# Kernel optimization log

Hardware: AMD Instinct MI355X
Metric: run time of the kernel (lower is better)

The kernel has to match this reference:

```python
import jax, jax.numpy as jnp
import numpy as np

B, C, L = 32, 64, 4096
PS, STRIDE = 16, 8
PC = (L - PS) // STRIDE + 1  # 511
HID = 64


def setup_inputs() -> dict:
    key = jax.random.key(0)
    k = jax.random.split(key, 5)
    X = jax.random.normal(k[0], (B, C, L), dtype=jnp.float32)
    W1 = jax.random.normal(k[1], (HID, PS), dtype=jnp.float32) * 0.05  # Conv1d(1,64,PS) weight
    b1 = jax.random.normal(k[2], (HID,), dtype=jnp.float32) * 0.05
    W2 = jax.random.normal(k[3], (2, HID), dtype=jnp.float32) * 0.05   # Conv1d(64,2,1) weight
    b2 = jax.random.normal(k[4], (2,), dtype=jnp.float32) * 0.05
    return {"X": X, "W1": W1, "b1": b1, "W2": W2, "b2": b2}


def reference(X, W1, b1, W2, b2):
    Bn, Cn, Ln = X.shape
    s_bias = (PS - 1) / 2.0
    # anchors: center of each patch along the sequence axis
    anchor = jnp.arange(PC, dtype=X.dtype) * STRIDE + 0.5 * (PS - 1)  # (PC,)

    # ---- OffsetPredictor: unfold into (B, C, PC, PS) sliding windows ----
    idx = jnp.arange(PC)[:, None] * STRIDE + jnp.arange(PS)[None, :]  # (PC, PS)
    patches = X[:, :, idx]  # (B, C, PC, PS)
    # Conv1d(1, HID, PS) over a length-PS window == dense matmul with W1
    h = jax.nn.gelu(jnp.einsum('bcps,ks->bcpk', patches, W1) + b1, approximate=False)
    off = jnp.einsum('bcpk,jk->bcpj', h, W2) + b2  # (B, C, PC, 2)
    off = off.transpose(0, 2, 1, 3)  # (B, PC, C, 2)

    # ---- BoxCoder.decode ----
    dx = off[..., 0]
    ds = jax.nn.relu(off[..., 1] + s_bias)
    ref = anchor[None, :, None]
    lo = jnp.clip((dx + ref - ds) / (Ln - 1), 0.0, 1.0)  # (B, PC, C)
    hi = jnp.clip((dx + ref + ds) / (Ln - 1), 0.0, 1.0)

    # ---- BoxCoder.meshgrid: linear interp from box endpoints (align_corners) ----
    t = jnp.arange(PS, dtype=X.dtype) / (PS - 1)  # (PS,)
    xs = lo[..., None] + (hi - lo)[..., None] * t  # (B, PC, C, PS), in [0,1]
    ys = jnp.arange(Cn, dtype=X.dtype) / (Cn - 1)  # (C,), in [0,1]

    # ---- grid_sample(img=(B,1,C,L), grid=(xs,ys)*2-1, bilinear, align_corners=True) ----
    ix = xs * (Ln - 1)                                            # (B, PC, C, PS)
    iy = jnp.broadcast_to(ys[None, None, :, None] * (Cn - 1), ix.shape)
    ix0 = jnp.floor(ix)
    iy0 = jnp.floor(iy)
    wx = ix - ix0
    wy = iy - iy0
    ix0i = jnp.clip(ix0.astype(jnp.int32), 0, Ln - 1)
    ix1i = jnp.clip(ix0i + 1, 0, Ln - 1)
    iy0i = jnp.clip(iy0.astype(jnp.int32), 0, Cn - 1)
    iy1i = jnp.clip(iy0i + 1, 0, Cn - 1)

    gather = jax.vmap(lambda x, r, c: x[r, c])  # over batch; x:(C,L)
    v00 = gather(X, iy0i, ix0i)
    v01 = gather(X, iy0i, ix1i)
    v10 = gather(X, iy1i, ix0i)
    v11 = gather(X, iy1i, ix1i)
    out = (v00 * (1 - wx) + v01 * wx) * (1 - wy) + (v10 * (1 - wx) + v11 * wx) * wy
    # (B, PC, C, PS) -> (B, C, PC, PS)
    return out.transpose(0, 2, 1, 3)
```

## Files before the change

kernel.cpp:

```cpp
#include <hip/hip_runtime.h>
#include <math.h>

#define L_    4096
#define PS_   16
#define STR_  8
#define PC_   511
#define HID_  64
#define NBLK_ 2048

typedef __bf16 bf16x8 __attribute__((ext_vector_type(8)));
typedef float  f32x4  __attribute__((ext_vector_type(4)));

__device__ __forceinline__ float gelu_fast(float x) {
    float u = x * x;
    float t = fmaf(u, 0.10294294f, 2.3022082f);
    float a = x * t;
    float e = __builtin_amdgcn_exp2f(a);
    float r = __builtin_amdgcn_rcpf(e + 1.0f);
    return fmaf(-x, r, x);
}

__device__ __forceinline__ bf16x8 load_frag(const float* __restrict__ p) {
    float4 v0 = *reinterpret_cast<const float4*>(p);
    float4 v1 = *reinterpret_cast<const float4*>(p + 4);
    bf16x8 r;
    r[0] = (__bf16)v0.x; r[1] = (__bf16)v0.y; r[2] = (__bf16)v0.z; r[3] = (__bf16)v0.w;
    r[4] = (__bf16)v1.x; r[5] = (__bf16)v1.y; r[6] = (__bf16)v1.z; r[7] = (__bf16)v1.w;
    return r;
}

__global__ __launch_bounds__(256, 4) void depatch_kernel(
    const float* __restrict__ X,
    const float* __restrict__ W1,
    const float* __restrict__ b1,
    const float* __restrict__ W2,
    const float* __restrict__ b2,
    float* __restrict__ out)
{
    __shared__ __attribute__((aligned(16))) float s_row[L_ + 32];

    const int tid = threadIdx.x;
    const int bc  = blockIdx.x;
    const float* xrow = X + (size_t)bc * L_;

    {
        const float4* src4 = reinterpret_cast<const float4*>(xrow);
        float4* dst4 = reinterpret_cast<float4*>(s_row);
        #pragma unroll
        for (int i = 0; i < 4; ++i) dst4[tid + 256 * i] = src4[tid + 256 * i];
        if (tid < 32) s_row[L_ + tid] = 0.0f;
    }

    const int l   = tid & 63;
    const int lr  = l & 15;
    const int lq  = l >> 4;
    const int lkb = lq * 8;

    bf16x8 afrag[4];
    f32x4  b1c[4];
    float  w2x[4][4], w2s[4][4];
    #pragma unroll
    for (int nb = 0; nb < 4; ++nb) {
        #pragma unroll
        for (int j = 0; j < 8; ++j) {
            int ks = lkb + j;
            afrag[nb][j] = (__bf16)((ks < PS_) ? W1[(nb * 16 + lr) * PS_ + ks] : 0.0f);
        }
        #pragma unroll
        for (int r = 0; r < 4; ++r) {
            int hid = nb * 16 + lq * 4 + r;
            b1c[nb][r] = b1[hid];
            w2x[nb][r] = W2[hid];
            w2s[nb][r] = W2[HID_ + hid];
        }
    }
    const float b20 = b2[0];
    const float b21 = b2[1];
    const float t0  = (float)lq * (4.0f / 15.0f);
    __syncthreads();

    const int wave = tid >> 6;
    float* obase = out + (size_t)bc * PC_ * PS_;
    const float* bbase = s_row + (size_t)(wave * 128 + lr + lq) * 8;

#define MLP_REDUCE(cA0, cA1, cA2, cA3, dxv, dsv)                         \
    {                                                                    \
        float dx0 = 0.0f, dx1 = 0.0f, ds0 = 0.0f, ds1 = 0.0f;            \
        _Pragma("unroll")                                                \
        for (int r = 0; r < 4; ++r) {                                    \
            float g0 = gelu_fast(cA0[r]);                                \
            float g1 = gelu_fast(cA1[r]);                                \
            float g2 = gelu_fast(cA2[r]);                                \
            float g3 = gelu_fast(cA3[r]);                                \
            dx0 = fmaf(g0, w2x[0][r], dx0);                              \
            dx0 = fmaf(g1, w2x[1][r], dx0);                              \
            dx1 = fmaf(g2, w2x[2][r], dx1);                              \
            dx1 = fmaf(g3, w2x[3][r], dx1);                              \
            ds0 = fmaf(g0, w2s[0][r], ds0);                              \
            ds0 = fmaf(g1, w2s[1][r], ds0);                              \
            ds1 = fmaf(g2, w2s[2][r], ds1);                              \
            ds1 = fmaf(g3, w2s[3][r], ds1);                              \
        }                                                                \
        float dx_ = dx0 + dx1, ds_ = ds0 + ds1;                          \
        dx_ += __shfl_xor(dx_, 16, 64);  ds_ += __shfl_xor(ds_, 16, 64); \
        dx_ += __shfl_xor(dx_, 32, 64);  ds_ += __shfl_xor(ds_, 32, 64); \
        dxv = dx_ + b20;  dsv = ds_ + b21;                               \
    }

#define SAMPLE_STORE(p, dxv, dsv)                                        \
    {                                                                    \
        const float refp = (float)((p) * STR_) + 7.5f;                   \
        const float d2   = fmaxf((dsv) + 7.5f, 0.0f);                    \
        const float aa   = (dxv) + refp;                                 \
        const float loi  = fminf(fmaxf(aa - d2, 0.0f), 4095.0f);         \
        const float hii  = fminf(fmaxf(aa + d2, 0.0f), 4095.0f);         \
        const float span = hii - loi;                                    \
        float4 o;                                                        \
        float* ov = reinterpret_cast<float*>(&o);                        \
        _Pragma("unroll")                                                \
        for (int si = 0; si < 4; ++si) {                                 \
            float t  = t0 + (float)si * (1.0f / 15.0f);                  \
            float ix = fmaf(span, t, loi);                               \
            float f  = floorf(ix);                                       \
            float wx = ix - f;                                           \
            int i0 = (int)f;                                             \
            float v0 = s_row[i0];                                        \
            float v1 = s_row[i0 + 1];        \
            ov[si] = fmaf(wx, v1 - v0, v0);                              \
        }                                                                \
        if ((p) < PC_)                                                   \
            *reinterpret_cast<float4*>(obase + (size_t)(p) * PS_ + lq * 4) = o; \
    }

    bf16x8 nA = load_frag(bbase);
    bf16x8 nB = load_frag(bbase + 128);

    #pragma unroll
    for (int i = 0; i < 4; ++i) {
        const bf16x8 cA = nA, cB = nB;
        if (i < 3) {
            nA = load_frag(bbase + (2 * i + 2) * 128);
            nB = load_frag(bbase + (2 * i + 3) * 128);
        }
        f32x4 a0 = __builtin_amdgcn_mfma_f32_16x16x32_bf16(afrag[0], cA, b1c[0], 0, 0, 0);
        f32x4 a1 = __builtin_amdgcn_mfma_f32_16x16x32_bf16(afrag[1], cA, b1c[1], 0, 0, 0);
        f32x4 a2 = __builtin_amdgcn_mfma_f32_16x16x32_bf16(afrag[2], cA, b1c[2], 0, 0, 0);
        f32x4 a3 = __builtin_amdgcn_mfma_f32_16x16x32_bf16(afrag[3], cA, b1c[3], 0, 0, 0);
        f32x4 q0 = __builtin_amdgcn_mfma_f32_16x16x32_bf16(afrag[0], cB, b1c[0], 0, 0, 0);
        f32x4 q1 = __builtin_amdgcn_mfma_f32_16x16x32_bf16(afrag[1], cB, b1c[1], 0, 0, 0);
        f32x4 q2 = __builtin_amdgcn_mfma_f32_16x16x32_bf16(afrag[2], cB, b1c[2], 0, 0, 0);
        f32x4 q3 = __builtin_amdgcn_mfma_f32_16x16x32_bf16(afrag[3], cB, b1c[3], 0, 0, 0);

        float dxA, dsA, dxB, dsB;
        MLP_REDUCE(a0, a1, a2, a3, dxA, dsA)
        MLP_REDUCE(q0, q1, q2, q3, dxB, dsB)

        const int pA = wave * 128 + (2 * i) * 16 + lr;
        const int pB = pA + 16;
        SAMPLE_STORE(pA, dxA, dsA)
        SAMPLE_STORE(pB, dxB, dsB)
    }
#undef MLP_REDUCE
#undef SAMPLE_STORE
}

extern "C" void kernel_launch(void* const* d_in, const int* in_sizes, int n_in,
                              void* d_out, int out_size, void* d_ws, size_t ws_size,
                              hipStream_t stream) {
    const float* X  = (const float*)d_in[0];
    const float* W1 = (const float*)d_in[1];
    const float* b1 = (const float*)d_in[2];
    const float* W2 = (const float*)d_in[3];
    const float* b2 = (const float*)d_in[4];
    float* out = (float*)d_out;

    depatch_kernel<<<dim3(NBLK_), dim3(256), 0, stream>>>(X, W1, b1, W2, b2, out);
}
```

Measured before the change: 130.2 us.

## Split fused kernel into MLP offset kernel and separate sampling kernel

Splits the single fused kernel into two launches. The first computes per-patch offsets with MFMA, reading X straight from global memory without shared memory, and writes (dx, ds) pairs to a workspace. The second stages each row in shared memory and does the bilinear sampling and the output store. The aim is to give each phase lighter register and shared-memory pressure, so occupancy and latency hiding improve. In exchange it adds a second launch, a workspace round trip, and a second full read of X.

```diff
diff --git a/kernel.cpp b/kernel.cpp
--- a/kernel.cpp
+++ b/kernel.cpp
@@ -7,6 +7,7 @@
 #define PC_   511
 #define HID_  64
 #define NBLK_ 2048
+#define WSTRIDE_ 512
 
 typedef __bf16 bf16x8 __attribute__((ext_vector_type(8)));
 typedef float  f32x4  __attribute__((ext_vector_type(4)));
@@ -20,36 +21,17 @@
     return fmaf(-x, r, x);
 }
 
-__device__ __forceinline__ bf16x8 load_frag(const float* __restrict__ p) {
-    float4 v0 = *reinterpret_cast<const float4*>(p);
-    float4 v1 = *reinterpret_cast<const float4*>(p + 4);
-    bf16x8 r;
-    r[0] = (__bf16)v0.x; r[1] = (__bf16)v0.y; r[2] = (__bf16)v0.z; r[3] = (__bf16)v0.w;
-    r[4] = (__bf16)v1.x; r[5] = (__bf16)v1.y; r[6] = (__bf16)v1.z; r[7] = (__bf16)v1.w;
-    return r;
-}
-
-__global__ __launch_bounds__(256, 4) void depatch_kernel(
+__global__ __launch_bounds__(256, 4) void mlp_kernel(
     const float* __restrict__ X,
     const float* __restrict__ W1,
     const float* __restrict__ b1,
     const float* __restrict__ W2,
     const float* __restrict__ b2,
-    float* __restrict__ out)
+    float2* __restrict__ ws)
 {
-    __shared__ __attribute__((aligned(16))) float s_row[L_ + 32];
-
     const int tid = threadIdx.x;
     const int bc  = blockIdx.x;
     const float* xrow = X + (size_t)bc * L_;
-
-    {
-        const float4* src4 = reinterpret_cast<const float4*>(xrow);
-        float4* dst4 = reinterpret_cast<float4*>(s_row);
-        #pragma unroll
-        for (int i = 0; i < 4; ++i) dst4[tid + 256 * i] = src4[tid + 256 * i];
-        if (tid < 32) s_row[L_ + tid] = 0.0f;
-    }
 
     const int l   = tid & 63;
     const int lr  = l & 15;
@@ -76,12 +58,20 @@
     }
     const float b20 = b2[0];
     const float b21 = b2[1];
-    const float t0  = (float)lq * (4.0f / 15.0f);
-    __syncthreads();
 
     const int wave = tid >> 6;
-    float* obase = out + (size_t)bc * PC_ * PS_;
-    const float* bbase = s_row + (size_t)(wave * 128 + lr + lq) * 8;
+    float2* wsrow = ws + (size_t)bc * WSTRIDE_;
+
+    auto ldfrag = [&](int g) -> bf16x8 {
+        int off = ((g << 4) + lr + lq) << 3;
+        off = min(off, L_ - 8);
+        float4 v0 = *reinterpret_cast<const float4*>(xrow + off);
+        float4 v1 = *reinterpret_cast<const float4*>(xrow + off + 4);
+        bf16x8 r;
+        r[0]=(__bf16)v0.x; r[1]=(__bf16)v0.y; r[2]=(__bf16)v0.z; r[3]=(__bf16)v0.w;
+        r[4]=(__bf16)v1.x; r[5]=(__bf16)v1.y; r[6]=(__bf16)v1.z; r[7]=(__bf16)v1.w;
+        return r;
+    };
 
 #define MLP_REDUCE(cA0, cA1, cA2, cA3, dxv, dsv)                         \
     {                                                                    \
@@ -107,40 +97,15 @@
         dxv = dx_ + b20;  dsv = ds_ + b21;                               \
     }
 
-#define SAMPLE_STORE(p, dxv, dsv)                                        \
-    {                                                                    \
-        const float refp = (float)((p) * STR_) + 7.5f;                   \
-        const float d2   = fmaxf((dsv) + 7.5f, 0.0f);                    \
-        const float aa   = (dxv) + refp;                                 \
-        const float loi  = fminf(fmaxf(aa - d2, 0.0f), 4095.0f);         \
-        const float hii  = fminf(fmaxf(aa + d2, 0.0f), 4095.0f);         \
-        const float span = hii - loi;                                    \
-        float4 o;                                                        \
-        float* ov = reinterpret_cast<float*>(&o);                        \
-        _Pragma("unroll")                                                \
-        for (int si = 0; si < 4; ++si) {                                 \
-            float t  = t0 + (float)si * (1.0f / 15.0f);                  \
-            float ix = fmaf(span, t, loi);                               \
-            float f  = floorf(ix);                                       \
-            float wx = ix - f;                                           \
-            int i0 = (int)f;                                             \
-            float v0 = s_row[i0];                                        \
-            float v1 = s_row[i0 + 1];        \
-            ov[si] = fmaf(wx, v1 - v0, v0);                              \
-        }                                                                \
-        if ((p) < PC_)                                                   \
-            *reinterpret_cast<float4*>(obase + (size_t)(p) * PS_ + lq * 4) = o; \
-    }
-
-    bf16x8 nA = load_frag(bbase);
-    bf16x8 nB = load_frag(bbase + 128);
+    bf16x8 nA = ldfrag(wave * 8 + 0);
+    bf16x8 nB = ldfrag(wave * 8 + 1);
 
     #pragma unroll
     for (int i = 0; i < 4; ++i) {
         const bf16x8 cA = nA, cB = nB;
         if (i < 3) {
-            nA = load_frag(bbase + (2 * i + 2) * 128);
-            nB = load_frag(bbase + (2 * i + 3) * 128);
+            nA = ldfrag(wave * 8 + 2 * i + 2);
+            nB = ldfrag(wave * 8 + 2 * i + 3);
         }
         f32x4 a0 = __builtin_amdgcn_mfma_f32_16x16x32_bf16(afrag[0], cA, b1c[0], 0, 0, 0);
         f32x4 a1 = __builtin_amdgcn_mfma_f32_16x16x32_bf16(afrag[1], cA, b1c[1], 0, 0, 0);
@@ -157,11 +122,79 @@
 
         const int pA = wave * 128 + (2 * i) * 16 + lr;
         const int pB = pA + 16;
-        SAMPLE_STORE(pA, dxA, dsA)
-        SAMPLE_STORE(pB, dxB, dsB)
+        if (lq == 0) {
+            if (pA < PC_) wsrow[pA] = make_float2(dxA, dsA);
+            if (pB < PC_) wsrow[pB] = make_float2(dxB, dsB);
+        }
     }
 #undef MLP_REDUCE
-#undef SAMPLE_STORE
+}
+
+__global__ __launch_bounds__(256, 4) void sample_kernel(
+    const float* __restrict__ X,
+    const float2* __restrict__ ws,
+    float* __restrict__ out)
+{
+    __shared__ __attribute__((aligned(16))) float s_row[L_ + 32];
+
+    const int tid = threadIdx.x;
+    const int bc  = blockIdx.x;
+    const float* xrow = X + (size_t)bc * L_;
+
+    const int l  = tid & 63;
+    const int lr = l & 15;
+    const int lq = l >> 4;
+    const int wave = tid >> 6;
+    const float2* wsrow = ws + (size_t)bc * WSTRIDE_;
+
+    float2 dd[8];
+    #pragma unroll
+    for (int gi = 0; gi < 8; ++gi) {
+        int p = wave * 128 + gi * 16 + lr;
+        dd[gi] = wsrow[min(p, PC_ - 1)];
+    }
+
+    {
+        const float4* src4 = reinterpret_cast<const float4*>(xrow);
+        float4* dst4 = reinterpret_cast<float4*>(s_row);
+        #pragma unroll
+        for (int i = 0; i < 4; ++i) dst4[tid + 256 * i] = src4[tid + 256 * i];
+        if (tid < 32) s_row[L_ + tid] = 0.0f;
+    }
+    __syncthreads();
+
+    const float t0 = (float)lq * (4.0f / 15.0f);
+    float* obase = out + (size_t)bc * PC_ * PS_;
+
+    #pragma unroll
+    for (int gi = 0; gi < 8; ++gi) {
+        const int p = wave * 128 + gi * 16 + lr;
+        const float dx = dd[gi].x;
+        const float ds = dd[gi].y;
+
+        const float refp = (float)(p * STR_) + 7.5f;
+        const float d2   = fmaxf(ds + 7.5f, 0.0f);
+        const float aa   = dx + refp;
+        const float loi  = fminf(fmaxf(aa - d2, 0.0f), 4095.0f);
+        const float hii  = fminf(fmaxf(aa + d2, 0.0f), 4095.0f);
+        const float span = hii - loi;
+
+        float4 o;
+        float* ov = reinterpret_cast<float*>(&o);
+        #pragma unroll
+        for (int si = 0; si < 4; ++si) {
+            float t  = t0 + (float)si * (1.0f / 15.0f);
+            float ix = fmaf(span, t, loi);
+            float f  = floorf(ix);
+            float wx = ix - f;
+            int i0 = (int)f;
+            float v0 = s_row[i0];
+            float v1 = s_row[i0 + 1];
+            ov[si] = fmaf(wx, v1 - v0, v0);
+        }
+        if (p < PC_)
+            *reinterpret_cast<float4*>(obase + (size_t)p * PS_ + lq * 4) = o;
+    }
 }
 
 extern "C" void kernel_launch(void* const* d_in, const int* in_sizes, int n_in,
@@ -173,6 +206,8 @@
     const float* W2 = (const float*)d_in[3];
     const float* b2 = (const float*)d_in[4];
     float* out = (float*)d_out;
-
-    depatch_kernel<<<dim3(NBLK_), dim3(256), 0, stream>>>(X, W1, b1, W2, b2, out);
-}
+    float2* ws = (float2*)d_ws;
+
+    mlp_kernel<<<dim3(NBLK_), dim3(256), 0, stream>>>(X, W1, b1, W2, b2, ws);
+    sample_kernel<<<dim3(NBLK_), dim3(256), 0, stream>>>(X, ws, out);
+}
```

New measurement: 144.9 us. 11.3% more time.
